# Performance work log

Measured on AMD Instinct MI355X. Metric: run time of the kernel, lower is better.

The kernel has to match this reference:

```python
import jax, jax.numpy as jnp
import numpy as np

D_K = 64
SCALE = 1.0 / np.sqrt(D_K).astype(np.float32)


def setup_inputs() -> dict:
    key = jax.random.key(0)
    kq, kk, kv = jax.random.split(key, 3)
    B, S, D = 4, 2048, 512
    q = jax.random.normal(kq, (B, S, D), dtype=jnp.float32)
    k = jax.random.normal(kk, (B, S, D), dtype=jnp.float32)
    v = jax.random.normal(kv, (B, S, D), dtype=jnp.float32)
    return {"q": q, "k": k, "v": v}


def reference(q, k, v):
    # n_head == 1: the per-head strided slices are the full tensors.
    # Original computes BOTH 'new_k' (scaled q@k^T) and 'new_v' (unscaled q@k^T);
    # note: v is never used in the original forward math (faithful reproduction).
    qk = jnp.einsum('bsd,btd->bst', q, k)           # [B, S, S]
    scores = qk * SCALE                              # new_k
    attn = jax.nn.softmax(scores, axis=2)            # softmax over dim 2
    # dropout with p=0.1 is identity in eval / deterministic reference
    out = jnp.matmul(attn, qk)                       # attn @ new_v -> [B, S, S]
    return out
```

## Files before the change

kernel.cpp:

```cpp
#include <hip/hip_runtime.h>
#include <hip/hip_bf16.h>
#include <stdint.h>


#define SS 2048
#define DD 512
#define BATCH 4
#define NTB 8

typedef __attribute__((ext_vector_type(8))) short short8;
typedef __attribute__((ext_vector_type(8))) _Float16 half8;
typedef __attribute__((ext_vector_type(4))) float floatx4;
typedef __attribute__((ext_vector_type(4))) float float4v;
typedef __attribute__((ext_vector_type(4))) unsigned int uintx4;

#define GLOBAL_AS const __attribute__((address_space(1)))
#define LDS_AS __attribute__((address_space(3)))

__device__ __forceinline__ uint32_t pk2h(float x, float y) {
    _Float16 hx = (_Float16)x, hy = (_Float16)y;
    union { _Float16 h; uint16_t u; } cx, cy;
    cx.h = hx; cy.h = hy;
    return (uint32_t)cx.u | ((uint32_t)cy.u << 16);
}
__device__ __forceinline__ float h2f(uint32_t ubits) {
    union { uint16_t u; _Float16 h; } c; c.u = (uint16_t)ubits; return (float)c.h;
}
__device__ __forceinline__ uint16_t f2h(float f) {
    union { _Float16 h; uint16_t u; } c; c.h = (_Float16)f; return c.u;
}

union PackU { uint32_t u[4]; short8 s8; };

__global__ __launch_bounds__(256) void prep_kernel(
    const float* __restrict__ Q, const float* __restrict__ K,
    uint16_t* __restrict__ qT, uint16_t* __restrict__ qH,
    uint16_t* __restrict__ kH)
{
    const int b   = blockIdx.z;
    const int tid = threadIdx.x;

    if (blockIdx.y >= 8) {
        const float* src = (blockIdx.y == 8) ? (K + (size_t)b * SS * DD)
                                             : (Q + (size_t)b * SS * DD);
        uint16_t* dst = (blockIdx.y == 8) ? (kH + (size_t)b * SS * DD)
                                          : (qH + (size_t)b * SS * DD);
        const int g0 = blockIdx.x * 256 + tid;
#pragma unroll
        for (int i = 0; i < 16; ++i) {
            const int g = g0 + i * 8192;
            const float4v* s4 = (const float4v*)(src + (size_t)g * 8);
            float4v x0 = s4[0], x1 = s4[1];
            PackU p;
            p.u[0] = pk2h(x0[0], x0[1]);
            p.u[1] = pk2h(x0[2], x0[3]);
            p.u[2] = pk2h(x1[0], x1[1]);
            p.u[3] = pk2h(x1[2], x1[3]);
            *(short8*)(dst + (size_t)g * 8) = p.s8;
        }
        return;
    }

    const int u0 = blockIdx.x * 64;
    const int d0 = blockIdx.y * 64;
    const float* qb = Q + (size_t)b * SS * DD;
    uint16_t* qTb = qT + (size_t)b * DD * SS;

    __shared__ uint16_t T[64 * 66];

    {
        const int r  = tid >> 2;
        const int c4 = (tid & 3) * 16;
        const float* src = qb + (size_t)(u0 + r) * DD + d0 + c4;
        float4v x0 = *(const float4v*)(src + 0);
        float4v x1 = *(const float4v*)(src + 4);
        float4v x2 = *(const float4v*)(src + 8);
        float4v x3 = *(const float4v*)(src + 12);
        uint32_t* tw = (uint32_t*)&T[r * 66 + c4];
        tw[0] = pk2h(x0[0], x0[1]); tw[1] = pk2h(x0[2], x0[3]);
        tw[2] = pk2h(x1[0], x1[1]); tw[3] = pk2h(x1[2], x1[3]);
        tw[4] = pk2h(x2[0], x2[1]); tw[5] = pk2h(x2[2], x2[3]);
        tw[6] = pk2h(x3[0], x3[1]); tw[7] = pk2h(x3[2], x3[3]);
    }
    __syncthreads();
#pragma unroll
    for (int p = 0; p < 2; ++p) {
        const int dl  = (tid >> 3) + p * 32;
        const int ul8 = (tid & 7) * 8;
        uint16_t t8[8];
#pragma unroll
        for (int j = 0; j < 8; ++j) t8[j] = T[(ul8 + j) * 66 + dl];
        PackU o;
        o.u[0] = (uint32_t)t8[0] | ((uint32_t)t8[1] << 16);
        o.u[1] = (uint32_t)t8[2] | ((uint32_t)t8[3] << 16);
        o.u[2] = (uint32_t)t8[4] | ((uint32_t)t8[5] << 16);
        o.u[3] = (uint32_t)t8[6] | ((uint32_t)t8[7] << 16);
        *(short8*)(&qTb[(size_t)(d0 + dl) * SS + u0 + ul8]) = o.s8;
    }
}

__global__ __launch_bounds__(512, 2) void gemm1_kernel(
    const uint16_t* __restrict__ qH, const uint16_t* __restrict__ kH,
    uint16_t* __restrict__ qk)
{
    const int b  = blockIdx.z;
    const int s0 = blockIdx.y * 256;
    const int t0 = blockIdx.x * 256;
    const uint16_t* ab = qH + (size_t)b * SS * DD;
    const uint16_t* bb = kH + (size_t)b * SS * DD;

    __shared__ uint16_t smem[65536];

    const int tid  = threadIdx.x;
    const int lane = tid & 63;
    const int wave = tid >> 6;
    const int wm   = wave >> 2;
    const int wn   = wave & 3;
    const int fm   = lane & 15;
    const int quad = lane >> 4;

    floatx4 acc[8][4];
#pragma unroll
    for (int i = 0; i < 8; ++i)
#pragma unroll
        for (int j = 0; j < 4; ++j)
            acc[i][j] = (floatx4)0.0f;

    const int sl0  = (quad ^ (fm & 7)) * 8;
    const int aoff = (wm * 128 + fm) * 64;
    const int boff = 32768 + (wn * 64 + fm) * 64;

    const int c0 = wave * 128 + lane;
    const int r0 = c0 >> 3;  const int l0 = ((c0 & 7) ^ (r0 & 7)) * 8;
    const int c1 = c0 + 64;
    const int r1 = c1 >> 3;  const int l1 = ((c1 & 7) ^ (r1 & 7)) * 8;
    const int ldsW = wave * 1024;

    auto STAGE_A = [&](int tt, int h) {
        uint16_t* base = &smem[(tt & 1) * 16384 + h * 8192 + ldsW];
        __builtin_amdgcn_global_load_lds(
            (GLOBAL_AS void*)(ab + (size_t)(s0 + h * 128 + r0) * DD + tt * 64 + l0),
            (LDS_AS void*)(base), 16, 0, 0);
        __builtin_amdgcn_global_load_lds(
            (GLOBAL_AS void*)(ab + (size_t)(s0 + h * 128 + r1) * DD + tt * 64 + l1),
            (LDS_AS void*)(base + 512), 16, 0, 0);
    };
    auto STAGE_B = [&](int tt, int h) {
        uint16_t* base = &smem[32768 + (tt & 1) * 16384 + h * 8192 + ldsW];
        __builtin_amdgcn_global_load_lds(
            (GLOBAL_AS void*)(bb + (size_t)(t0 + h * 128 + r0) * DD + tt * 64 + l0),
            (LDS_AS void*)(base), 16, 0, 0);
        __builtin_amdgcn_global_load_lds(
            (GLOBAL_AS void*)(bb + (size_t)(t0 + h * 128 + r1) * DD + tt * 64 + l1),
            (LDS_AS void*)(base + 512), 16, 0, 0);
    };

    STAGE_A(0, 0); STAGE_A(0, 1); STAGE_B(0, 0); STAGE_B(0, 1);
    STAGE_B(1, 0); STAGE_B(1, 1);
    asm volatile("s_waitcnt vmcnt(4)" ::: "memory");
    __builtin_amdgcn_s_barrier();

    half8 aF[4], aF2[4], bF[4][2];

    for (int t = 0; t < NTB; ++t) {
        const int abase = (t & 1) * 16384;
        const int bbase = (t & 1) * 16384;

#pragma unroll
        for (int nt = 0; nt < 4; ++nt) {
            bF[nt][0] = *(const half8*)&smem[bbase + boff + nt * 1024 + sl0];
            bF[nt][1] = *(const half8*)&smem[bbase + boff + nt * 1024 + (sl0 ^ 32)];
        }
#pragma unroll
        for (int m = 0; m < 4; ++m)
            aF[m] = *(const half8*)&smem[abase + aoff + m * 1024 + sl0];
        if (t + 1 < NTB) STAGE_A(t + 1, 0);
        __builtin_amdgcn_s_barrier();
        asm volatile("s_waitcnt lgkmcnt(0)" ::: "memory");
        __builtin_amdgcn_s_setprio(1);
#pragma unroll
        for (int m = 0; m < 4; ++m)
#pragma unroll
            for (int nt = 0; nt < 4; ++nt)
                acc[m][nt] = __builtin_amdgcn_mfma_f32_16x16x32_f16(aF[m], bF[nt][0], acc[m][nt], 0, 0, 0);
        __builtin_amdgcn_s_setprio(0);
        __builtin_amdgcn_s_barrier();

#pragma unroll
        for (int m = 0; m < 4; ++m)
            aF2[m] = *(const half8*)&smem[abase + aoff + (m + 4) * 1024 + sl0];
        if (t + 1 < NTB) STAGE_A(t + 1, 1);
        __builtin_amdgcn_s_barrier();
        asm volatile("s_waitcnt lgkmcnt(0)" ::: "memory");
        __builtin_amdgcn_s_setprio(1);
#pragma unroll
        for (int m = 0; m < 4; ++m)
#pragma unroll
            for (int nt = 0; nt < 4; ++nt)
                acc[m + 4][nt] = __builtin_amdgcn_mfma_f32_16x16x32_f16(aF2[m], bF[nt][0], acc[m + 4][nt], 0, 0, 0);
        __builtin_amdgcn_s_setprio(0);
        __builtin_amdgcn_s_barrier();

#pragma unroll
        for (int m = 0; m < 4; ++m)
            aF[m] = *(const half8*)&smem[abase + aoff + m * 1024 + (sl0 ^ 32)];
        if (t + 2 < NTB) STAGE_B(t + 2, 0);
        __builtin_amdgcn_s_barrier();
        asm volatile("s_waitcnt lgkmcnt(0)" ::: "memory");
        __builtin_amdgcn_s_setprio(1);
#pragma unroll
        for (int m = 0; m < 4; ++m)
#pragma unroll
            for (int nt = 0; nt < 4; ++nt)
                acc[m][nt] = __builtin_amdgcn_mfma_f32_16x16x32_f16(aF[m], bF[nt][1], acc[m][nt], 0, 0, 0);
        __builtin_amdgcn_s_setprio(0);
        __builtin_amdgcn_s_barrier();

#pragma unroll
        for (int m = 0; m < 4; ++m)
            aF2[m] = *(const half8*)&smem[abase + aoff + (m + 4) * 1024 + (sl0 ^ 32)];
        if (t + 2 < NTB) {
            STAGE_B(t + 2, 1);
            asm volatile("s_waitcnt vmcnt(4)" ::: "memory");
        } else {
            asm volatile("s_waitcnt vmcnt(0)" ::: "memory");
        }
        __builtin_amdgcn_s_barrier();
        asm volatile("s_waitcnt lgkmcnt(0)" ::: "memory");
        __builtin_amdgcn_s_setprio(1);
#pragma unroll
        for (int m = 0; m < 4; ++m)
#pragma unroll
            for (int nt = 0; nt < 4; ++nt)
                acc[m + 4][nt] = __builtin_amdgcn_mfma_f32_16x16x32_f16(aF2[m], bF[nt][1], acc[m + 4][nt], 0, 0, 0);
        __builtin_amdgcn_s_setprio(0);
        __builtin_amdgcn_s_barrier();
    }

    uint16_t* ob = qk + (size_t)b * SS * SS;
#pragma unroll
    for (int mt = 0; mt < 8; ++mt) {
#pragma unroll
        for (int nt = 0; nt < 4; ++nt) {
            const int srow = s0 + wm * 128 + mt * 16 + quad * 4;
            const int tcol = t0 + wn * 64 + nt * 16 + fm;
#pragma unroll
            for (int reg = 0; reg < 4; ++reg)
                ob[(size_t)(srow + reg) * SS + tcol] = f2h(acc[mt][nt][reg]);
        }
    }
}

__global__ __launch_bounds__(256) void softmax_inplace(uint16_t* __restrict__ qk)
{
    const size_t row = blockIdx.x;
    uint16_t* x = qk + row * SS;
    const int tid  = threadIdx.x;
    const int lane = tid & 63;
    const int wave = tid >> 6;

    uintx4 raw = *(const uintx4*)(x + tid * 8);
    float v[8];
#pragma unroll
    for (int i = 0; i < 4; ++i) {
        uint32_t u = raw[i];
        v[2 * i]     = h2f(u & 0xffffu) * 0.125f;
        v[2 * i + 1] = h2f(u >> 16) * 0.125f;
    }
    float m = v[0];
#pragma unroll
    for (int j = 1; j < 8; ++j) m = fmaxf(m, v[j]);
#pragma unroll
    for (int off = 1; off < 64; off <<= 1) m = fmaxf(m, __shfl_xor(m, off, 64));
    __shared__ float red[8];
    if (lane == 0) red[wave] = m;
    __syncthreads();
    m = fmaxf(fmaxf(red[0], red[1]), fmaxf(red[2], red[3]));

    float s = 0.f;
#pragma unroll
    for (int j = 0; j < 8; ++j) { v[j] = __expf(v[j] - m); s += v[j]; }
#pragma unroll
    for (int off = 1; off < 64; off <<= 1) s += __shfl_xor(s, off, 64);
    if (lane == 0) red[4 + wave] = s;
    __syncthreads();
    s = (red[4] + red[5]) + (red[6] + red[7]);
    const float inv = 1.0f / s;
#pragma unroll
    for (int i = 0; i < 4; ++i)
        raw[i] = pk2h(v[2 * i] * inv, v[2 * i + 1] * inv);
    *(uintx4*)(x + tid * 8) = raw;
}

__global__ __launch_bounds__(256, 2) void gemm2a_kernel(
    const uint16_t* __restrict__ attn, const uint16_t* __restrict__ qT,
    uint16_t* __restrict__ tmp)
{
    const int b  = blockIdx.z;
    const int s0 = blockIdx.y * 128;
    const int t0 = blockIdx.x * 128;
    const uint16_t* ab = attn + (size_t)b * SS * SS;
    const uint16_t* bb = qT   + (size_t)b * DD * SS;

    __shared__ uint16_t As[2 * 128 * 32];
    __shared__ uint16_t Bs[2 * 128 * 32];

    const int tid  = threadIdx.x;
    const int lane = tid & 63;
    const int wave = tid >> 6;
    const int wm = wave >> 1, wn = wave & 1;
    const int fm = lane & 15, quad = lane >> 4;

    floatx4 acc[4][4];
#pragma unroll
    for (int i = 0; i < 4; ++i)
#pragma unroll
        for (int j = 0; j < 4; ++j)
            acc[i][j] = (floatx4)0.0f;

    const int c0i = wave * 128 + lane;
    const int c1i = c0i + 64;
    const int rA0 = c0i >> 2, pA0 = c0i & 3;
    const int rA1 = c1i >> 2, pA1 = c1i & 3;
    const int ldsOff0 = (wave * 128) * 8;
    const int ldsOff1 = (wave * 128 + 64) * 8;

    for (int k0 = 0; k0 < SS; k0 += 64) {
        __syncthreads();
#pragma unroll
        for (int ks = 0; ks < 2; ++ks) {
            const int kc = k0 + ks * 32;
            uint16_t* asub = &As[ks * 4096];
            uint16_t* bsub = &Bs[ks * 4096];
            __builtin_amdgcn_global_load_lds(
                (GLOBAL_AS void*)(ab + (size_t)(s0 + rA0) * SS + kc + pA0 * 8),
                (LDS_AS void*)(asub + ldsOff0), 16, 0, 0);
            __builtin_amdgcn_global_load_lds(
                (GLOBAL_AS void*)(ab + (size_t)(s0 + rA1) * SS + kc + pA1 * 8),
                (LDS_AS void*)(asub + ldsOff1), 16, 0, 0);
            __builtin_amdgcn_global_load_lds(
                (GLOBAL_AS void*)(bb + (size_t)(t0 + rA0) * SS + kc + pA0 * 8),
                (LDS_AS void*)(bsub + ldsOff0), 16, 0, 0);
            __builtin_amdgcn_global_load_lds(
                (GLOBAL_AS void*)(bb + (size_t)(t0 + rA1) * SS + kc + pA1 * 8),
                (LDS_AS void*)(bsub + ldsOff1), 16, 0, 0);
        }
        __syncthreads();

#pragma unroll
        for (int ks = 0; ks < 2; ++ks) {
            half8 fa[4], fb[4];
#pragma unroll
            for (int mt = 0; mt < 4; ++mt)
                fa[mt] = *(const half8*)(&As[ks * 4096 + (wm * 64 + mt * 16 + fm) * 32 + quad * 8]);
#pragma unroll
            for (int nt = 0; nt < 4; ++nt)
                fb[nt] = *(const half8*)(&Bs[ks * 4096 + (wn * 64 + nt * 16 + fm) * 32 + quad * 8]);
#pragma unroll
            for (int mt = 0; mt < 4; ++mt)
#pragma unroll
                for (int nt = 0; nt < 4; ++nt)
                    acc[mt][nt] = __builtin_amdgcn_mfma_f32_16x16x32_f16(fa[mt], fb[nt], acc[mt][nt], 0, 0, 0);
        }
    }

    uint16_t* tb = tmp + (size_t)b * SS * DD;
#pragma unroll
    for (int mt = 0; mt < 4; ++mt) {
#pragma unroll
        for (int nt = 0; nt < 4; ++nt) {
            const int srow = s0 + wm * 64 + mt * 16 + quad * 4;
            const int tcol = t0 + wn * 64 + nt * 16 + fm;
#pragma unroll
            for (int reg = 0; reg < 4; ++reg)
                tb[(size_t)(srow + reg) * DD + tcol] = f2h(acc[mt][nt][reg]);
        }
    }
}

__global__ __launch_bounds__(512, 2) void gemm2b_kernel(
    const uint16_t* __restrict__ tmp, const uint16_t* __restrict__ kH,
    float* __restrict__ out)
{
    const int b  = blockIdx.z;
    const int s0 = blockIdx.y * 256;
    const int t0 = blockIdx.x * 256;
    const uint16_t* ab = tmp + (size_t)b * SS * DD;
    const uint16_t* bb = kH  + (size_t)b * SS * DD;

    __shared__ uint16_t smem[65536];

    const int tid  = threadIdx.x;
    const int lane = tid & 63;
    const int wave = tid >> 6;
    const int wm   = wave >> 2;
    const int wn   = wave & 3;
    const int fm   = lane & 15;
    const int quad = lane >> 4;

    floatx4 acc[8][4];
#pragma unroll
    for (int i = 0; i < 8; ++i)
#pragma unroll
        for (int j = 0; j < 4; ++j)
            acc[i][j] = (floatx4)0.0f;

    const int sl0  = (quad ^ (fm & 7)) * 8;
    const int aoff = (wm * 128 + fm) * 64;
    const int boff = 32768 + (wn * 64 + fm) * 64;

    const int c0 = wave * 128 + lane;
    const int r0 = c0 >> 3;  const int l0 = ((c0 & 7) ^ (r0 & 7)) * 8;
    const int c1 = c0 + 64;
    const int r1 = c1 >> 3;  const int l1 = ((c1 & 7) ^ (r1 & 7)) * 8;
    const int ldsW = wave * 1024;

    auto STAGE_A = [&](int tt, int h) {
        uint16_t* base = &smem[(tt & 1) * 16384 + h * 8192 + ldsW];
        __builtin_amdgcn_global_load_lds(
            (GLOBAL_AS void*)(ab + (size_t)(s0 + h * 128 + r0) * DD + tt * 64 + l0),
            (LDS_AS void*)(base), 16, 0, 0);
        __builtin_amdgcn_global_load_lds(
            (GLOBAL_AS void*)(ab + (size_t)(s0 + h * 128 + r1) * DD + tt * 64 + l1),
            (LDS_AS void*)(base + 512), 16, 0, 0);
    };
    auto STAGE_B = [&](int tt, int h) {
        uint16_t* base = &smem[32768 + (tt & 1) * 16384 + h * 8192 + ldsW];
        __builtin_amdgcn_global_load_lds(
            (GLOBAL_AS void*)(bb + (size_t)(t0 + h * 128 + r0) * DD + tt * 64 + l0),
            (LDS_AS void*)(base), 16, 0, 0);
        __builtin_amdgcn_global_load_lds(
            (GLOBAL_AS void*)(bb + (size_t)(t0 + h * 128 + r1) * DD + tt * 64 + l1),
            (LDS_AS void*)(base + 512), 16, 0, 0);
    };

    STAGE_A(0, 0); STAGE_A(0, 1); STAGE_B(0, 0); STAGE_B(0, 1);
    STAGE_B(1, 0); STAGE_B(1, 1);
    asm volatile("s_waitcnt vmcnt(4)" ::: "memory");
    __builtin_amdgcn_s_barrier();

    half8 aF[4], aF2[4], bF[4][2];

    for (int t = 0; t < NTB; ++t) {
        const int abase = (t & 1) * 16384;
        const int bbase = (t & 1) * 16384;

#pragma unroll
        for (int nt = 0; nt < 4; ++nt) {
            bF[nt][0] = *(const half8*)&smem[bbase + boff + nt * 1024 + sl0];
            bF[nt][1] = *(const half8*)&smem[bbase + boff + nt * 1024 + (sl0 ^ 32)];
        }
#pragma unroll
        for (int m = 0; m < 4; ++m)
            aF[m] = *(const half8*)&smem[abase + aoff + m * 1024 + sl0];
        if (t + 1 < NTB) STAGE_A(t + 1, 0);
        __builtin_amdgcn_s_barrier();
        asm volatile("s_waitcnt lgkmcnt(0)" ::: "memory");
        __builtin_amdgcn_s_setprio(1);
#pragma unroll
        for (int m = 0; m < 4; ++m)
#pragma unroll
            for (int nt = 0; nt < 4; ++nt)
                acc[m][nt] = __builtin_amdgcn_mfma_f32_16x16x32_f16(aF[m], bF[nt][0], acc[m][nt], 0, 0, 0);
        __builtin_amdgcn_s_setprio(0);
        __builtin_amdgcn_s_barrier();

#pragma unroll
        for (int m = 0; m < 4; ++m)
            aF2[m] = *(const half8*)&smem[abase + aoff + (m + 4) * 1024 + sl0];
        if (t + 1 < NTB) STAGE_A(t + 1, 1);
        __builtin_amdgcn_s_barrier();
        asm volatile("s_waitcnt lgkmcnt(0)" ::: "memory");
        __builtin_amdgcn_s_setprio(1);
#pragma unroll
        for (int m = 0; m < 4; ++m)
#pragma unroll
            for (int nt = 0; nt < 4; ++nt)
                acc[m + 4][nt] = __builtin_amdgcn_mfma_f32_16x16x32_f16(aF2[m], bF[nt][0], acc[m + 4][nt], 0, 0, 0);
        __builtin_amdgcn_s_setprio(0);
        __builtin_amdgcn_s_barrier();

#pragma unroll
        for (int m = 0; m < 4; ++m)
            aF[m] = *(const half8*)&smem[abase + aoff + m * 1024 + (sl0 ^ 32)];
        if (t + 2 < NTB) STAGE_B(t + 2, 0);
        __builtin_amdgcn_s_barrier();
        asm volatile("s_waitcnt lgkmcnt(0)" ::: "memory");
        __builtin_amdgcn_s_setprio(1);
#pragma unroll
        for (int m = 0; m < 4; ++m)
#pragma unroll
            for (int nt = 0; nt < 4; ++nt)
                acc[m][nt] = __builtin_amdgcn_mfma_f32_16x16x32_f16(aF[m], bF[nt][1], acc[m][nt], 0, 0, 0);
        __builtin_amdgcn_s_setprio(0);
        __builtin_amdgcn_s_barrier();

#pragma unroll
        for (int m = 0; m < 4; ++m)
            aF2[m] = *(const half8*)&smem[abase + aoff + (m + 4) * 1024 + (sl0 ^ 32)];
        if (t + 2 < NTB) {
            STAGE_B(t + 2, 1);
            asm volatile("s_waitcnt vmcnt(4)" ::: "memory");
        } else {
            asm volatile("s_waitcnt vmcnt(0)" ::: "memory");
        }
        __builtin_amdgcn_s_barrier();
        asm volatile("s_waitcnt lgkmcnt(0)" ::: "memory");
        __builtin_amdgcn_s_setprio(1);
#pragma unroll
        for (int m = 0; m < 4; ++m)
#pragma unroll
            for (int nt = 0; nt < 4; ++nt)
                acc[m + 4][nt] = __builtin_amdgcn_mfma_f32_16x16x32_f16(aF2[m], bF[nt][1], acc[m + 4][nt], 0, 0, 0);
        __builtin_amdgcn_s_setprio(0);
        __builtin_amdgcn_s_barrier();
    }

    float* ob = out + (size_t)b * SS * SS;
#pragma unroll
    for (int mt = 0; mt < 8; ++mt) {
#pragma unroll
        for (int nt = 0; nt < 4; ++nt) {
            const int srow = s0 + wm * 128 + mt * 16 + quad * 4;
            const int tcol = t0 + wn * 64 + nt * 16 + fm;
#pragma unroll
            for (int reg = 0; reg < 4; ++reg)
                ob[(size_t)(srow + reg) * SS + tcol] = acc[mt][nt][reg];
        }
    }
}

extern "C" void kernel_launch(void* const* d_in, const int* in_sizes, int n_in,
                              void* d_out, int out_size, void* d_ws, size_t ws_size,
                              hipStream_t stream) {
    const float* q = (const float*)d_in[0];
    const float* k = (const float*)d_in[1];
    float* out = (float*)d_out;

    uint16_t* qk  = (uint16_t*)d_ws;
    uint16_t* qT  = qk + (size_t)BATCH * SS * SS;
    uint16_t* qH  = qT + (size_t)BATCH * DD * SS;
    uint16_t* kH  = qH + (size_t)BATCH * SS * DD;
    uint16_t* tmp = kH + (size_t)BATCH * SS * DD;

    prep_kernel<<<dim3(32, 10, BATCH), 256, 0, stream>>>(q, k, qT, qH, kH);
    gemm1_kernel<<<dim3(SS / 256, SS / 256, BATCH), 512, 0, stream>>>(qH, kH, qk);
    softmax_inplace<<<dim3(BATCH * SS), 256, 0, stream>>>(qk);
    gemm2a_kernel<<<dim3(DD / 128, SS / 128, BATCH), 256, 0, stream>>>(qk, qT, tmp);
    gemm2b_kernel<<<dim3(SS / 256, SS / 256, BATCH), 512, 0, stream>>>(tmp, kH, out);
}
```

Measured before the change: 204.9 us.

## Double-buffer gemm2a with XOR-swizzled LDS and 512-thread blocks

Rewrites the attn@q GEMM kernel to use 8 waves per 128x128 tile instead of 4. It stages 64-wide K tiles into double-buffered LDS with global_load_lds and issues the prefetch of tile t+2 between the two MFMA halves. LDS rows use an XOR swizzle to avoid bank conflicts, and s_setprio raises MFMA priority. The aim is to hide global-load latency and cut barrier stalls, at the cost of more manual waitcnt and barrier ordering that must stay correct.

Measured after the change: 186.7 us. 8.9% less time.

```diff
diff --git a/kernel.cpp b/kernel.cpp
--- a/kernel.cpp
+++ b/kernel.cpp
@@ -7,6 +7,7 @@
 #define DD 512
 #define BATCH 4
 #define NTB 8
+#define NT2A 32
 
 typedef __attribute__((ext_vector_type(8))) short short8;
 typedef __attribute__((ext_vector_type(8))) _Float16 half8;
@@ -292,7 +293,7 @@
     *(uintx4*)(x + tid * 8) = raw;
 }
 
-__global__ __launch_bounds__(256, 2) void gemm2a_kernel(
+__global__ __launch_bounds__(512, 2) void gemm2a_kernel(
     const uint16_t* __restrict__ attn, const uint16_t* __restrict__ qT,
     uint16_t* __restrict__ tmp)
 {
@@ -302,78 +303,107 @@
     const uint16_t* ab = attn + (size_t)b * SS * SS;
     const uint16_t* bb = qT   + (size_t)b * DD * SS;
 
-    __shared__ uint16_t As[2 * 128 * 32];
-    __shared__ uint16_t Bs[2 * 128 * 32];
+    __shared__ uint16_t smem[32768];
 
     const int tid  = threadIdx.x;
     const int lane = tid & 63;
     const int wave = tid >> 6;
-    const int wm = wave >> 1, wn = wave & 1;
-    const int fm = lane & 15, quad = lane >> 4;
-
-    floatx4 acc[4][4];
+    const int wm   = wave >> 2;
+    const int wn   = wave & 3;
+    const int fm   = lane & 15;
+    const int quad = lane >> 4;
+
+    floatx4 acc[4][2];
 #pragma unroll
     for (int i = 0; i < 4; ++i)
 #pragma unroll
-        for (int j = 0; j < 4; ++j)
+        for (int j = 0; j < 2; ++j)
             acc[i][j] = (floatx4)0.0f;
 
-    const int c0i = wave * 128 + lane;
-    const int c1i = c0i + 64;
-    const int rA0 = c0i >> 2, pA0 = c0i & 3;
-    const int rA1 = c1i >> 2, pA1 = c1i & 3;
-    const int ldsOff0 = (wave * 128) * 8;
-    const int ldsOff1 = (wave * 128 + 64) * 8;
-
-    for (int k0 = 0; k0 < SS; k0 += 64) {
-        __syncthreads();
-#pragma unroll
-        for (int ks = 0; ks < 2; ++ks) {
-            const int kc = k0 + ks * 32;
-            uint16_t* asub = &As[ks * 4096];
-            uint16_t* bsub = &Bs[ks * 4096];
-            __builtin_amdgcn_global_load_lds(
-                (GLOBAL_AS void*)(ab + (size_t)(s0 + rA0) * SS + kc + pA0 * 8),
-                (LDS_AS void*)(asub + ldsOff0), 16, 0, 0);
-            __builtin_amdgcn_global_load_lds(
-                (GLOBAL_AS void*)(ab + (size_t)(s0 + rA1) * SS + kc + pA1 * 8),
-                (LDS_AS void*)(asub + ldsOff1), 16, 0, 0);
-            __builtin_amdgcn_global_load_lds(
-                (GLOBAL_AS void*)(bb + (size_t)(t0 + rA0) * SS + kc + pA0 * 8),
-                (LDS_AS void*)(bsub + ldsOff0), 16, 0, 0);
-            __builtin_amdgcn_global_load_lds(
-                (GLOBAL_AS void*)(bb + (size_t)(t0 + rA1) * SS + kc + pA1 * 8),
-                (LDS_AS void*)(bsub + ldsOff1), 16, 0, 0);
-        }
-        __syncthreads();
-
-#pragma unroll
-        for (int ks = 0; ks < 2; ++ks) {
-            half8 fa[4], fb[4];
-#pragma unroll
-            for (int mt = 0; mt < 4; ++mt)
-                fa[mt] = *(const half8*)(&As[ks * 4096 + (wm * 64 + mt * 16 + fm) * 32 + quad * 8]);
-#pragma unroll
-            for (int nt = 0; nt < 4; ++nt)
-                fb[nt] = *(const half8*)(&Bs[ks * 4096 + (wn * 64 + nt * 16 + fm) * 32 + quad * 8]);
-#pragma unroll
-            for (int mt = 0; mt < 4; ++mt)
-#pragma unroll
-                for (int nt = 0; nt < 4; ++nt)
-                    acc[mt][nt] = __builtin_amdgcn_mfma_f32_16x16x32_f16(fa[mt], fb[nt], acc[mt][nt], 0, 0, 0);
-        }
+    const int sl0  = (quad ^ (fm & 7)) * 8;
+    const int aoff = (wm * 64 + fm) * 64;
+    const int boff = 16384 + (wn * 32 + fm) * 64;
+
+    const int r0 = tid >> 3;
+    const int l0 = (((tid & 7) ^ (r0 & 7))) * 8;
+    const int r1 = r0 + 64;
+    const int l1 = (((tid & 7) ^ (r1 & 7))) * 8;
+    const int ldsW = wave * 512;
+
+    auto STAGE_A = [&](int tt) {
+        uint16_t* base = &smem[(tt & 1) * 8192 + ldsW];
+        __builtin_amdgcn_global_load_lds(
+            (GLOBAL_AS void*)(ab + (size_t)(s0 + r0) * SS + tt * 64 + l0),
+            (LDS_AS void*)(base), 16, 0, 0);
+        __builtin_amdgcn_global_load_lds(
+            (GLOBAL_AS void*)(ab + (size_t)(s0 + r1) * SS + tt * 64 + l1),
+            (LDS_AS void*)(base + 4096), 16, 0, 0);
+    };
+    auto STAGE_B = [&](int tt) {
+        uint16_t* base = &smem[16384 + (tt & 1) * 8192 + ldsW];
+        __builtin_amdgcn_global_load_lds(
+            (GLOBAL_AS void*)(bb + (size_t)(t0 + r0) * SS + tt * 64 + l0),
+            (LDS_AS void*)(base), 16, 0, 0);
+        __builtin_amdgcn_global_load_lds(
+            (GLOBAL_AS void*)(bb + (size_t)(t0 + r1) * SS + tt * 64 + l1),
+            (LDS_AS void*)(base + 4096), 16, 0, 0);
+    };
+
+    STAGE_A(0); STAGE_B(0); STAGE_A(1); STAGE_B(1);
+    asm volatile("s_waitcnt vmcnt(4)" ::: "memory");
+    __builtin_amdgcn_s_barrier();
+
+    half8 aF[4][2], bF[2][2];
+
+    for (int t = 0; t < NT2A; ++t) {
+        const int buf = (t & 1) * 8192;
+
+#pragma unroll
+        for (int m = 0; m < 4; ++m) {
+            aF[m][0] = *(const half8*)&smem[buf + aoff + m * 1024 + sl0];
+            aF[m][1] = *(const half8*)&smem[buf + aoff + m * 1024 + (sl0 ^ 32)];
+        }
+#pragma unroll
+        for (int n = 0; n < 2; ++n) {
+            bF[n][0] = *(const half8*)&smem[buf + boff + n * 1024 + sl0];
+            bF[n][1] = *(const half8*)&smem[buf + boff + n * 1024 + (sl0 ^ 32)];
+        }
+        asm volatile("s_waitcnt lgkmcnt(0)" ::: "memory");
+        __builtin_amdgcn_s_setprio(1);
+#pragma unroll
+        for (int m = 0; m < 4; ++m)
+#pragma unroll
+            for (int n = 0; n < 2; ++n)
+                acc[m][n] = __builtin_amdgcn_mfma_f32_16x16x32_f16(aF[m][0], bF[n][0], acc[m][n], 0, 0, 0);
+        __builtin_amdgcn_s_setprio(0);
+        __builtin_amdgcn_s_barrier();
+
+        if (t + 2 < NT2A) {
+            STAGE_A(t + 2); STAGE_B(t + 2);
+            asm volatile("s_waitcnt vmcnt(4)" ::: "memory");
+        } else {
+            asm volatile("s_waitcnt vmcnt(0)" ::: "memory");
+        }
+        __builtin_amdgcn_s_barrier();
+        __builtin_amdgcn_s_setprio(1);
+#pragma unroll
+        for (int m = 0; m < 4; ++m)
+#pragma unroll
+            for (int n = 0; n < 2; ++n)
+                acc[m][n] = __builtin_amdgcn_mfma_f32_16x16x32_f16(aF[m][1], bF[n][1], acc[m][n], 0, 0, 0);
+        __builtin_amdgcn_s_setprio(0);
     }
 
     uint16_t* tb = tmp + (size_t)b * SS * DD;
 #pragma unroll
     for (int mt = 0; mt < 4; ++mt) {
 #pragma unroll
-        for (int nt = 0; nt < 4; ++nt) {
-            const int srow = s0 + wm * 64 + mt * 16 + quad * 4;
-            const int tcol = t0 + wn * 64 + nt * 16 + fm;
+        for (int n = 0; n < 2; ++n) {
+            const int srw  = s0 + wm * 64 + mt * 16 + quad * 4;
+            const int tcol = t0 + wn * 32 + n * 16 + fm;
 #pragma unroll
             for (int reg = 0; reg < 4; ++reg)
-                tb[(size_t)(srow + reg) * DD + tcol] = f2h(acc[mt][nt][reg]);
+                tb[(size_t)(srw + reg) * DD + tcol] = f2h(acc[mt][n][reg]);
         }
     }
 }
@@ -546,6 +576,6 @@
     prep_kernel<<<dim3(32, 10, BATCH), 256, 0, stream>>>(q, k, qT, qH, kH);
     gemm1_kernel<<<dim3(SS / 256, SS / 256, BATCH), 512, 0, stream>>>(qH, kH, qk);
     softmax_inplace<<<dim3(BATCH * SS), 256, 0, stream>>>(qk);
-    gemm2a_kernel<<<dim3(DD / 128, SS / 128, BATCH), 256, 0, stream>>>(qk, qT, tmp);
+    gemm2a_kernel<<<dim3(DD / 128, SS / 128, BATCH), 512, 0, stream>>>(qk, qT, tmp);
     gemm2b_kernel<<<dim3(SS / 256, SS / 256, BATCH), 512, 0, stream>>>(tmp, kH, out);
 }
```
